# Kernel optimization log

Measured on AMD Instinct MI355X. Metric: run time of the kernel, lower is better.

Reference implementation:

```python
import jax, jax.numpy as jnp
import numpy as np

N, E = 50000, 800000
IN, HID, OUT, K = 500, 128, 128, 10
BN_EPS = 1e-5


def _encode(x, src, dst, norm, n, W_in, b_in, gam, high_pass, bn_scale, bn_shift, W_up, b_up):
    # input projection (dropout_p = 0 -> identity)
    h = x @ W_in + b_in  # [N, HID]

    def prop(t):
        # symmetric-normalized sparse matvec: (D^-1/2 A D^-1/2) t
        return jax.ops.segment_sum(norm[:, None] * t[src], dst, num_segments=n)

    def step(carry, g):
        t, acc = carry
        acc = acc + g * t
        pt = prop(t)
        # low-pass basis: A_hat^k x ; high-pass basis: (I - A_hat)^k x
        t = (t - pt) if high_pass else pt
        return (t, acc), None

    (_, acc), _ = jax.lax.scan(step, (h, jnp.zeros_like(h)), gam)

    # BatchNorm1d over the node axis (training-mode batch statistics)
    mu = acc.mean(axis=0)
    var = acc.var(axis=0)
    hn = (acc - mu) * jax.lax.rsqrt(var + BN_EPS) * bn_scale + bn_shift
    z = hn @ W_up + b_up
    return jax.nn.relu(z)  # act_fn='relu' (PolyGCL default)


def setup_inputs() -> dict:
    key = jax.random.key(0)
    ks = jax.random.split(key, 4)
    x = jax.random.normal(ks[0], (N, IN), dtype=jnp.float32)
    edge_index = jax.random.randint(ks[1], (2, E), 0, N, dtype=jnp.int32)
    W_in = jax.random.normal(ks[2], (IN, HID), dtype=jnp.float32) * (1.0 / np.sqrt(IN))
    b_in = jnp.zeros((HID,), dtype=jnp.float32)
    # low-pass: decreasing coefficients; high-pass: increasing (PolyGCL init scheme)
    gamma_L = jnp.linspace(2.0, 0.0, K + 1, dtype=jnp.float32)
    gamma_H = jnp.linspace(0.0, 2.0, K + 1, dtype=jnp.float32)
    bn_scale = jnp.ones((HID,), dtype=jnp.float32)
    bn_shift = jnp.zeros((HID,), dtype=jnp.float32)
    W_up = jax.random.normal(ks[3], (HID, OUT), dtype=jnp.float32) * (1.0 / np.sqrt(HID))
    b_up = jnp.zeros((OUT,), dtype=jnp.float32)
    return {"x": x, "edge_index": edge_index, "W_in": W_in, "b_in": b_in,
            "gamma_L": gamma_L, "gamma_H": gamma_H,
            "bn_scale": bn_scale, "bn_shift": bn_shift,
            "W_up": W_up, "b_up": b_up}


def reference(x, edge_index, W_in, b_in, gamma_L, gamma_H, bn_scale, bn_shift, W_up, b_up):
    n = x.shape[0]
    src, dst = edge_index[0], edge_index[1]
    deg = jax.ops.segment_sum(jnp.ones(src.shape, dtype=x.dtype), dst, num_segments=n)
    dinv = jax.lax.rsqrt(jnp.maximum(deg, 1.0))
    norm = dinv[src] * dinv[dst]  # [E]
    Z_L = _encode(x, src, dst, norm, n, W_in, b_in, gamma_L, False, bn_scale, bn_shift, W_up, b_up)
    Z_H = _encode(x, src, dst, norm, n, W_in, b_in, gamma_H, True, bn_scale, bn_shift, W_up, b_up)
    return (Z_L, Z_H)
```

## Files before the change

kernel.cpp:

```cpp
#include <hip/hip_runtime.h>
#include <hip/hip_fp16.h>

#define HIDF 128

typedef float v4f __attribute__((ext_vector_type(4)));
typedef _Float16 half8 __attribute__((ext_vector_type(8)));
typedef float f32x4 __attribute__((ext_vector_type(4)));
struct alignas(8) half4 { __half2 lo, hi; };

static inline int cdiv(int a, int b) { return (a + b - 1) / b; }
static inline size_t alup(size_t b) { return (b + 255) & ~(size_t)255; }

__global__ void k_deg(const int* __restrict__ dst, int E, int* __restrict__ deg) {
    int i = blockIdx.x * blockDim.x + threadIdx.x;
    if (i < E) atomicAdd(&deg[dst[i]], 1);
}

__global__ void k_coef(const float* __restrict__ gL, const float* __restrict__ gH, int K,
                       float* __restrict__ cL, float* __restrict__ cH) {
    if (threadIdx.x == 0 && blockIdx.x == 0) {
        for (int j = 0; j <= K; ++j) {
            double s = 0.0;
            double C = 1.0;
            for (int k = j; k <= K; ++k) {
                s += (double)gH[k] * C;
                C = C * (double)(k + 1) / (double)(k + 1 - j);
            }
            cH[j] = (j & 1) ? (float)(-s) : (float)s;
            cL[j] = gL[j];
        }
    }
}

__global__ __launch_bounds__(256) void k_scan1(const int* __restrict__ deg, int N,
                                               int* __restrict__ bsum,
                                               float* __restrict__ dinv) {
    __shared__ int ls[256];
    int tid = threadIdx.x;
    int i = blockIdx.x * 256 + tid;
    int v = 0;
    if (i < N) {
        v = deg[i];
        dinv[i] = rsqrtf(fmaxf((float)v, 1.0f));
    }
    ls[tid] = v;
    __syncthreads();
    for (int off = 128; off > 0; off >>= 1) {
        if (tid < off) ls[tid] += ls[tid + off];
        __syncthreads();
    }
    if (tid == 0) bsum[blockIdx.x] = ls[0];
}

__global__ __launch_bounds__(1024) void k_scan2(int* __restrict__ bsum, int nb) {
    __shared__ int ls[1024];
    int tid = threadIdx.x;
    int v = (tid < nb) ? bsum[tid] : 0;
    ls[tid] = v;
    __syncthreads();
    for (int off = 1; off < 1024; off <<= 1) {
        int t = (tid >= off) ? ls[tid - off] : 0;
        __syncthreads();
        ls[tid] += t;
        __syncthreads();
    }
    if (tid < nb) bsum[tid] = ls[tid] - v;
}

__global__ __launch_bounds__(256) void k_scan3(const int* __restrict__ deg,
                                               const int* __restrict__ bsum, int N,
                                               int* __restrict__ row_ptr) {
    __shared__ int ls[256];
    int tid = threadIdx.x;
    int i = blockIdx.x * 256 + tid;
    int v = (i < N) ? deg[i] : 0;
    ls[tid] = v;
    __syncthreads();
    for (int off = 1; off < 256; off <<= 1) {
        int t = (tid >= off) ? ls[tid - off] : 0;
        __syncthreads();
        ls[tid] += t;
        __syncthreads();
    }
    if (i <= N) row_ptr[i] = bsum[blockIdx.x] + ls[tid] - v;
}

__global__ __launch_bounds__(1024) void k_scan(const int* __restrict__ deg, int N,
                                               int* __restrict__ row_ptr,
                                               float* __restrict__ dinv) {
    __shared__ int ls[1024];
    int tid = threadIdx.x;
    int chunk = (N + 1023) / 1024;
    int start = tid * chunk;
    int end = min(start + chunk, N);
    int s = 0;
    for (int i = start; i < end; ++i) {
        int d = deg[i];
        s += d;
        dinv[i] = rsqrtf(fmaxf((float)d, 1.0f));
    }
    ls[tid] = s;
    __syncthreads();
    for (int off = 1; off < 1024; off <<= 1) {
        int v = (tid >= off) ? ls[tid - off] : 0;
        __syncthreads();
        ls[tid] += v;
        __syncthreads();
    }
    int run = ls[tid] - s;
    for (int i = start; i < end; ++i) {
        row_ptr[i] = run;
        run += deg[i];
    }
    if (tid == 1023) row_ptr[N] = run;
}

__global__ void k_scatter(const int* __restrict__ src, const int* __restrict__ dst, int E,
                          const int* __restrict__ row_ptr, int* __restrict__ fill,
                          const float* __restrict__ dinv, int* __restrict__ csr_src,
                          float* __restrict__ csr_w) {
    int i = blockIdx.x * blockDim.x + threadIdx.x;
    if (i < E) {
        int s = src[i], d = dst[i];
        int pos = row_ptr[d] + atomicAdd(&fill[d], 1);
        csr_src[pos] = s;
        csr_w[pos] = dinv[s] * dinv[d];
    }
}

__global__ __launch_bounds__(512) void k_wprep(const float* __restrict__ W, int Kdim, int KP,
                                               _Float16* __restrict__ Wh,
                                               _Float16* __restrict__ Wl) {
    int i = blockIdx.x * blockDim.x + threadIdx.x;
    int total = 128 * KP;
    if (i >= total) return;
    int n = i / KP;
    int k = i - n * KP;
    float w = (k < Kdim) ? W[(long)k * HIDF + n] : 0.0f;
    _Float16 h = (_Float16)w;
    _Float16 l = (_Float16)(w - (float)h);
    Wh[(long)n * KP + k] = h;
    Wl[(long)n * KP + k] = l;
}

__global__ __launch_bounds__(512) void k_gemm_in_mfma(
    const float* __restrict__ X, const _Float16* __restrict__ Wh,
    const _Float16* __restrict__ Wl, const float* __restrict__ b, __half* __restrict__ U0,
    int M, int Kdim, int KP) {
    __shared__ _Float16 Ah[128][40];
    __shared__ _Float16 Al[128][40];
    __shared__ _Float16 Bh[128][40];
    __shared__ _Float16 Bl[128][40];
    int tid = threadIdx.x;
    int lane = tid & 63;
    int wid = tid >> 6;
    int wr = wid >> 1;
    int wc = wid & 1;
    int lr = lane & 15;
    int kq = lane >> 4;
    int kof = kq * 8;
    int row0 = blockIdx.x * 128;
    int sm = tid >> 2;
    int kk = (tid & 3) * 8;
    bool k4ok = ((Kdim & 3) == 0);

    f32x4 acc[2][4] = {};

    for (int k0 = 0; k0 < KP; k0 += 32) {
        *(half8*)&Bh[sm][kk] = *(const half8*)&Wh[(long)sm * KP + k0 + kk];
        *(half8*)&Bl[sm][kk] = *(const half8*)&Wl[(long)sm * KP + k0 + kk];
        {
            int r = row0 + sm;
            int gk = k0 + kk;
            half8 hv, lv;
            if (r < M && (gk + 8) <= Kdim && k4ok) {
                float4 v0 = *(const float4*)&X[(long)r * Kdim + gk];
                float4 v1 = *(const float4*)&X[(long)r * Kdim + gk + 4];
                float xs[8] = {v0.x, v0.y, v0.z, v0.w, v1.x, v1.y, v1.z, v1.w};
#pragma unroll
                for (int j = 0; j < 8; ++j) {
                    _Float16 h = (_Float16)xs[j];
                    hv[j] = h;
                    lv[j] = (_Float16)(xs[j] - (float)h);
                }
            } else {
#pragma unroll
                for (int j = 0; j < 8; ++j) {
                    float x = (r < M && (gk + j) < Kdim) ? X[(long)r * Kdim + gk + j] : 0.0f;
                    _Float16 h = (_Float16)x;
                    hv[j] = h;
                    lv[j] = (_Float16)(x - (float)h);
                }
            }
            *(half8*)&Ah[sm][kk] = hv;
            *(half8*)&Al[sm][kk] = lv;
        }
        __syncthreads();

        half8 a_h0 = *(const half8*)&Ah[wr * 32 + lr][kof];
        half8 a_h1 = *(const half8*)&Ah[wr * 32 + 16 + lr][kof];
        half8 a_l0 = *(const half8*)&Al[wr * 32 + lr][kof];
        half8 a_l1 = *(const half8*)&Al[wr * 32 + 16 + lr][kof];
#pragma unroll
        for (int cg = 0; cg < 4; ++cg) {
            half8 b_h = *(const half8*)&Bh[wc * 64 + cg * 16 + lr][kof];
            half8 b_l = *(const half8*)&Bl[wc * 64 + cg * 16 + lr][kof];
            acc[0][cg] = __builtin_amdgcn_mfma_f32_16x16x32_f16(a_h0, b_h, acc[0][cg], 0, 0, 0);
            acc[1][cg] = __builtin_amdgcn_mfma_f32_16x16x32_f16(a_h1, b_h, acc[1][cg], 0, 0, 0);
            acc[0][cg] = __builtin_amdgcn_mfma_f32_16x16x32_f16(a_l0, b_h, acc[0][cg], 0, 0, 0);
            acc[1][cg] = __builtin_amdgcn_mfma_f32_16x16x32_f16(a_l1, b_h, acc[1][cg], 0, 0, 0);
            acc[0][cg] = __builtin_amdgcn_mfma_f32_16x16x32_f16(a_h0, b_l, acc[0][cg], 0, 0, 0);
            acc[1][cg] = __builtin_amdgcn_mfma_f32_16x16x32_f16(a_h1, b_l, acc[1][cg], 0, 0, 0);
        }
        __syncthreads();
    }

    float bb[4];
#pragma unroll
    for (int cg = 0; cg < 4; ++cg) bb[cg] = b[wc * 64 + cg * 16 + lr];
#pragma unroll
    for (int i = 0; i < 2; ++i) {
#pragma unroll
        for (int j = 0; j < 4; ++j) {
            int r = row0 + wr * 32 + i * 16 + kq * 4 + j;
            if (r < M) {
#pragma unroll
                for (int cg = 0; cg < 4; ++cg) {
                    int n = wc * 64 + cg * 16 + lr;
                    U0[(long)r * HIDF + n] = __float2half(acc[i][cg][j] + bb[cg]);
                }
            }
        }
    }
}

__global__ __launch_bounds__(512) void k_gemm_up_mfma(
    const float* __restrict__ accL, const float* __restrict__ accH,
    const _Float16* __restrict__ Wh, const _Float16* __restrict__ Wl,
    const float* __restrict__ bias, const float* __restrict__ a_mul,
    const float* __restrict__ aaW, float* __restrict__ out, int M) {
    int enc = blockIdx.y;
    const float* A = enc ? accH : accL;
    float* O = out + (size_t)enc * M * HIDF;
    __shared__ _Float16 Ah[128][40];
    __shared__ _Float16 Al[128][40];
    __shared__ _Float16 Bh[128][40];
    __shared__ _Float16 Bl[128][40];
    __shared__ float ams[128];
    int tid = threadIdx.x;
    int lane = tid & 63;
    int wid = tid >> 6;
    int wr = wid >> 1;
    int wc = wid & 1;
    int lr = lane & 15;
    int kq = lane >> 4;
    int kof = kq * 8;
    int row0 = blockIdx.x * 128;
    int sm = tid >> 2;
    int kk = (tid & 3) * 8;
    if (tid < 128) ams[tid] = a_mul[enc * 128 + tid];
    __syncthreads();

    f32x4 acc[2][4] = {};

    for (int k0 = 0; k0 < 128; k0 += 32) {
        *(half8*)&Bh[sm][kk] = *(const half8*)&Wh[(long)sm * 128 + k0 + kk];
        *(half8*)&Bl[sm][kk] = *(const half8*)&Wl[(long)sm * 128 + k0 + kk];
        {
            int r = row0 + sm;
            half8 hv, lv;
            if (r < M) {
                float4 v0 = *(const float4*)&A[(long)r * 128 + k0 + kk];
                float4 v1 = *(const float4*)&A[(long)r * 128 + k0 + kk + 4];
                float xs[8] = {v0.x, v0.y, v0.z, v0.w, v1.x, v1.y, v1.z, v1.w};
#pragma unroll
                for (int j = 0; j < 8; ++j) {
                    float sv = xs[j] * ams[k0 + kk + j];
                    _Float16 h = (_Float16)sv;
                    hv[j] = h;
                    lv[j] = (_Float16)(sv - (float)h);
                }
            } else {
#pragma unroll
                for (int j = 0; j < 8; ++j) { hv[j] = (_Float16)0.f; lv[j] = (_Float16)0.f; }
            }
            *(half8*)&Ah[sm][kk] = hv;
            *(half8*)&Al[sm][kk] = lv;
        }
        __syncthreads();

        half8 a_h0 = *(const half8*)&Ah[wr * 32 + lr][kof];
        half8 a_h1 = *(const half8*)&Ah[wr * 32 + 16 + lr][kof];
        half8 a_l0 = *(const half8*)&Al[wr * 32 + lr][kof];
        half8 a_l1 = *(const half8*)&Al[wr * 32 + 16 + lr][kof];
#pragma unroll
        for (int cg = 0; cg < 4; ++cg) {
            half8 b_h = *(const half8*)&Bh[wc * 64 + cg * 16 + lr][kof];
            half8 b_l = *(const half8*)&Bl[wc * 64 + cg * 16 + lr][kof];
            acc[0][cg] = __builtin_amdgcn_mfma_f32_16x16x32_f16(a_h0, b_h, acc[0][cg], 0, 0, 0);
            acc[1][cg] = __builtin_amdgcn_mfma_f32_16x16x32_f16(a_h1, b_h, acc[1][cg], 0, 0, 0);
            acc[0][cg] = __builtin_amdgcn_mfma_f32_16x16x32_f16(a_l0, b_h, acc[0][cg], 0, 0, 0);
            acc[1][cg] = __builtin_amdgcn_mfma_f32_16x16x32_f16(a_l1, b_h, acc[1][cg], 0, 0, 0);
            acc[0][cg] = __builtin_amdgcn_mfma_f32_16x16x32_f16(a_h0, b_l, acc[0][cg], 0, 0, 0);
            acc[1][cg] = __builtin_amdgcn_mfma_f32_16x16x32_f16(a_h1, b_l, acc[1][cg], 0, 0, 0);
        }
        __syncthreads();
    }

    float bb[4];
#pragma unroll
    for (int cg = 0; cg < 4; ++cg) {
        int n = wc * 64 + cg * 16 + lr;
        bb[cg] = bias[n] + aaW[enc * 128 + n];
    }
#pragma unroll
    for (int i = 0; i < 2; ++i) {
#pragma unroll
        for (int j = 0; j < 4; ++j) {
            int r = row0 + wr * 32 + i * 16 + kq * 4 + j;
            if (r < M) {
#pragma unroll
                for (int cg = 0; cg < 4; ++cg) {
                    int n = wc * 64 + cg * 16 + lr;
                    O[(long)r * HIDF + n] = fmaxf(acc[i][cg][j] + bb[cg], 0.0f);
                }
            }
        }
    }
}

__global__ __launch_bounds__(512) void k_gemm_in_f(
    const float* __restrict__ X, const float* __restrict__ W, const float* __restrict__ b,
    float* __restrict__ H, float* __restrict__ accL, float* __restrict__ accH,
    const float* __restrict__ cL, const float* __restrict__ cH, int M, int Kdim) {
    const int BK = 20;
    __shared__ float As[BK][132];
    __shared__ float Bs[BK][128];
    int tid = threadIdx.x;
    int tx = tid & 31, ty = tid >> 5;
    int row0 = blockIdx.x * 128;
    float acc[8][4] = {};
    for (int k0 = 0; k0 < Kdim; k0 += BK) {
        for (int l = tid; l < 640; l += 512) {
            int m = l / 5, q = l % 5;
            int r = row0 + m;
            float4 v = {0.f, 0.f, 0.f, 0.f};
            if (r < M) v = *(const float4*)&X[(long)r * Kdim + k0 + q * 4];
            As[q * 4 + 0][m] = v.x;
            As[q * 4 + 1][m] = v.y;
            As[q * 4 + 2][m] = v.z;
            As[q * 4 + 3][m] = v.w;
        }
        for (int l = tid; l < 640; l += 512) {
            int k = l >> 5, n = (l & 31) * 4;
            *(float4*)&Bs[k][n] = *(const float4*)&W[(long)(k0 + k) * 128 + n];
        }
        __syncthreads();
#pragma unroll
        for (int k = 0; k < BK; ++k) {
            float4 a0 = *(const float4*)&As[k][ty * 8];
            float4 a1 = *(const float4*)&As[k][ty * 8 + 4];
            float4 bb = *(const float4*)&Bs[k][tx * 4];
            float a[8] = {a0.x, a0.y, a0.z, a0.w, a1.x, a1.y, a1.z, a1.w};
#pragma unroll
            for (int i = 0; i < 8; ++i) {
                acc[i][0] += a[i] * bb.x;
                acc[i][1] += a[i] * bb.y;
                acc[i][2] += a[i] * bb.z;
                acc[i][3] += a[i] * bb.w;
            }
        }
        __syncthreads();
    }
    float g0 = cL[0], h0 = cH[0];
    float4 bias = *(const float4*)&b[tx * 4];
    float bv[4] = {bias.x, bias.y, bias.z, bias.w};
#pragma unroll
    for (int i = 0; i < 8; ++i) {
        int r = row0 + ty * 8 + i;
        if (r < M) {
            long idx = (long)r * 128 + tx * 4;
            float4 vh;
            float* ph = (float*)&vh;
#pragma unroll
            for (int j = 0; j < 4; ++j) ph[j] = acc[i][j] + bv[j];
            *(float4*)&H[idx] = vh;
            float4 vl = {g0 * vh.x, g0 * vh.y, g0 * vh.z, g0 * vh.w};
            float4 vv = {h0 * vh.x, h0 * vh.y, h0 * vh.z, h0 * vh.w};
            *(float4*)&accL[idx] = vl;
            *(float4*)&accH[idx] = vv;
        }
    }
}

__global__ __launch_bounds__(256) void k_prop_h(
    const int* __restrict__ row_ptr, const int* __restrict__ csr_src,
    const float* __restrict__ csr_w, const __half* __restrict__ t_in,
    __half* __restrict__ t_out, int N) {
    int tid = threadIdx.x;
    int lane = tid & 63;
    int wid = tid >> 6;
    int slot = lane >> 4;
    int l4 = lane & 15;
    int node = blockIdx.x * 16 + wid * 4 + slot;
    if (node >= N) return;
    int e0 = row_ptr[node], e1 = row_ptr[node + 1];
    float acc[8] = {};
    int e = e0;
    int nb = (e1 - e0) >> 3;

    int idxA[8];
    float wA[8];
    if (nb > 0) {
#pragma unroll
        for (int q = 0; q < 8; ++q) {
            idxA[q] = csr_src[e + q];
            wA[q] = csr_w[e + q];
        }
    }
    for (int bb = 0; bb < nb; ++bb) {
        half8 v[8];
#pragma unroll
        for (int q = 0; q < 8; ++q)
            v[q] = *(const half8*)&t_in[(long)idxA[q] * HIDF + l4 * 8];
        int en = e + 8;
        bool more = (bb + 1 < nb);
        int idxB[8];
        float wB[8];
        if (more) {
#pragma unroll
            for (int q = 0; q < 8; ++q) {
                idxB[q] = csr_src[en + q];
                wB[q] = csr_w[en + q];
            }
        }
#pragma unroll
        for (int q = 0; q < 8; ++q) {
#pragma unroll
            for (int f = 0; f < 8; ++f) acc[f] += wA[q] * (float)v[q][f];
        }
        if (more) {
#pragma unroll
            for (int q = 0; q < 8; ++q) {
                idxA[q] = idxB[q];
                wA[q] = wB[q];
            }
        }
        e = en;
    }
    for (; e < e1; ++e) {
        int i0 = csr_src[e];
        float w0 = csr_w[e];
        half8 v = *(const half8*)&t_in[(long)i0 * HIDF + l4 * 8];
#pragma unroll
        for (int f = 0; f < 8; ++f) acc[f] += w0 * (float)v[f];
    }
    half8 o;
#pragma unroll
    for (int f = 0; f < 8; ++f) o[f] = (_Float16)acc[f];
    *(half8*)&t_out[(long)node * HIDF + l4 * 8] = o;
}

__global__ __launch_bounds__(256) void k_prop(
    const int* __restrict__ row_ptr, const int* __restrict__ csr_src,
    const float* __restrict__ csr_w, const float* __restrict__ t_in,
    float* __restrict__ t_out, float* __restrict__ accL, float* __restrict__ accH,
    const float* __restrict__ cL, const float* __restrict__ cH, int j, int N, int write_t) {
    int wave = threadIdx.x >> 6;
    int lane = threadIdx.x & 63;
    int half = lane >> 5;
    int l5 = lane & 31;
    int node = blockIdx.x * 4 + wave;
    if (node >= N) return;
    int e0 = row_ptr[node], e1 = row_ptr[node + 1];
    float sx = 0.f, sy = 0.f, sz = 0.f, sw = 0.f;
    int e = e0 + half;
    for (; e + 6 < e1; e += 8) {
        int i0 = csr_src[e], i1 = csr_src[e + 2], i2 = csr_src[e + 4], i3 = csr_src[e + 6];
        float w0 = csr_w[e], w1 = csr_w[e + 2], w2 = csr_w[e + 4], w3 = csr_w[e + 6];
        float4 v0 = *(const float4*)&t_in[(long)i0 * HIDF + l5 * 4];
        float4 v1 = *(const float4*)&t_in[(long)i1 * HIDF + l5 * 4];
        float4 v2 = *(const float4*)&t_in[(long)i2 * HIDF + l5 * 4];
        float4 v3 = *(const float4*)&t_in[(long)i3 * HIDF + l5 * 4];
        sx += w0 * v0.x + w1 * v1.x + w2 * v2.x + w3 * v3.x;
        sy += w0 * v0.y + w1 * v1.y + w2 * v2.y + w3 * v3.y;
        sz += w0 * v0.z + w1 * v1.z + w2 * v2.z + w3 * v3.z;
        sw += w0 * v0.w + w1 * v1.w + w2 * v2.w + w3 * v3.w;
    }
    for (; e < e1; e += 2) {
        int i0 = csr_src[e];
        float w0 = csr_w[e];
        float4 v0 = *(const float4*)&t_in[(long)i0 * HIDF + l5 * 4];
        sx += w0 * v0.x;
        sy += w0 * v0.y;
        sz += w0 * v0.z;
        sw += w0 * v0.w;
    }
    sx += __shfl_xor(sx, 32);
    sy += __shfl_xor(sy, 32);
    sz += __shfl_xor(sz, 32);
    sw += __shfl_xor(sw, 32);
    if (half == 0) {
        long base = (long)node * HIDF + l5 * 4;
        if (write_t) {
            float4 o = {sx, sy, sz, sw};
            *(float4*)&t_out[base] = o;
        }
        float gL = cL[j], gH = cH[j];
        float4 aL = *(const float4*)&accL[base];
        float4 aH = *(const float4*)&accH[base];
        aL.x += gL * sx; aL.y += gL * sy; aL.z += gL * sz; aL.w += gL * sw;
        aH.x += gH * sx; aH.y += gH * sy; aH.z += gH * sz; aH.w += gH * sw;
        *(float4*)&accL[base] = aL;
        *(float4*)&accH[base] = aH;
    }
}

__global__ __launch_bounds__(256) void k_combine_h2(
    const __half* __restrict__ tb, long tstride, int K, float* __restrict__ accL,
    float* __restrict__ accH, const float* __restrict__ cL, const float* __restrict__ cH,
    int N, float* __restrict__ sums) {
    int tid = threadIdx.x;
    int fg = tid & 15;
    int rg = tid >> 4;
    int lane = tid & 63;
    int wid = tid >> 6;
    float s1[8] = {}, s2[8] = {}, s3[8] = {}, s4[8] = {};

    if (K == 10) {
        float gl[11], gh[11];
#pragma unroll
        for (int j = 0; j < 11; ++j) {
            gl[j] = cL[j];
            gh[j] = cH[j];
        }
        for (long r = (long)blockIdx.x * 16 + rg; r < N; r += (long)gridDim.x * 16) {
            const __half* p = tb + r * HIDF + fg * 8;
            half8 v[11];
#pragma unroll
            for (int j = 0; j < 11; ++j) v[j] = *(const half8*)(p + (long)j * tstride);
            float aL[8] = {}, aH[8] = {};
#pragma unroll
            for (int j = 0; j < 11; ++j) {
#pragma unroll
                for (int e = 0; e < 8; ++e) {
                    float t = (float)v[j][e];
                    aL[e] += gl[j] * t;
                    aH[e] += gh[j] * t;
                }
            }
            long base = r * HIDF + fg * 8;
            float4 o0 = {aL[0], aL[1], aL[2], aL[3]};
            float4 o1 = {aL[4], aL[5], aL[6], aL[7]};
            float4 o2 = {aH[0], aH[1], aH[2], aH[3]};
            float4 o3 = {aH[4], aH[5], aH[6], aH[7]};
            *(float4*)&accL[base] = o0;
            *(float4*)&accL[base + 4] = o1;
            *(float4*)&accH[base] = o2;
            *(float4*)&accH[base + 4] = o3;
#pragma unroll
            for (int e = 0; e < 8; ++e) {
                s1[e] += aL[e];
                s2[e] += aL[e] * aL[e];
                s3[e] += aH[e];
                s4[e] += aH[e] * aH[e];
            }
        }
    } else {
        for (long r = (long)blockIdx.x * 16 + rg; r < N; r += (long)gridDim.x * 16) {
            const __half* p = tb + r * HIDF + fg * 8;
            float aL[8] = {}, aH[8] = {};
            for (int j = 0; j <= K; ++j) {
                half8 v = *(const half8*)(p + (long)j * tstride);
                float gL = cL[j], gH = cH[j];
#pragma unroll
                for (int e = 0; e < 8; ++e) {
                    float t = (float)v[e];
                    aL[e] += gL * t;
                    aH[e] += gH * t;
                }
            }
            long base = r * HIDF + fg * 8;
            float4 o0 = {aL[0], aL[1], aL[2], aL[3]};
            float4 o1 = {aL[4], aL[5], aL[6], aL[7]};
            float4 o2 = {aH[0], aH[1], aH[2], aH[3]};
            float4 o3 = {aH[4], aH[5], aH[6], aH[7]};
            *(float4*)&accL[base] = o0;
            *(float4*)&accL[base + 4] = o1;
            *(float4*)&accH[base] = o2;
            *(float4*)&accH[base + 4] = o3;
#pragma unroll
            for (int e = 0; e < 8; ++e) {
                s1[e] += aL[e];
                s2[e] += aL[e] * aL[e];
                s3[e] += aH[e];
                s4[e] += aH[e] * aH[e];
            }
        }
    }

#pragma unroll
    for (int e = 0; e < 8; ++e) {
        s1[e] += __shfl_xor(s1[e], 16); s1[e] += __shfl_xor(s1[e], 32);
        s2[e] += __shfl_xor(s2[e], 16); s2[e] += __shfl_xor(s2[e], 32);
        s3[e] += __shfl_xor(s3[e], 16); s3[e] += __shfl_xor(s3[e], 32);
        s4[e] += __shfl_xor(s4[e], 16); s4[e] += __shfl_xor(s4[e], 32);
    }
    __shared__ float ls[4][16][32];
    if (lane < 16) {
#pragma unroll
        for (int e = 0; e < 8; ++e) {
            ls[wid][lane][e] = s1[e];
            ls[wid][lane][8 + e] = s2[e];
            ls[wid][lane][16 + e] = s3[e];
            ls[wid][lane][24 + e] = s4[e];
        }
    }
    __syncthreads();
    for (int idx = tid; idx < 512; idx += 256) {
        int f16i = idx >> 5, j = idx & 31;
        float v = ls[0][f16i][j] + ls[1][f16i][j] + ls[2][f16i][j] + ls[3][f16i][j];
        int stat = j >> 3, e = j & 7;
        atomicAdd(&sums[stat * 128 + f16i * 8 + e], v);
    }
}

__global__ __launch_bounds__(256) void k_stats(const float* __restrict__ accL,
                                               const float* __restrict__ accH, int N,
                                               float* __restrict__ sums) {
    int tid = threadIdx.x;
    int l5 = tid & 31;
    int g = tid >> 5;
    float4 l1 = {0, 0, 0, 0}, l2 = {0, 0, 0, 0}, h1 = {0, 0, 0, 0}, h2 = {0, 0, 0, 0};
    for (int r = blockIdx.x * 8 + g; r < N; r += gridDim.x * 8) {
        float4 v = *(const float4*)&accL[(long)r * HIDF + l5 * 4];
        l1.x += v.x; l1.y += v.y; l1.z += v.z; l1.w += v.w;
        l2.x += v.x * v.x; l2.y += v.y * v.y; l2.z += v.z * v.z; l2.w += v.w * v.w;
        float4 u = *(const float4*)&accH[(long)r * HIDF + l5 * 4];
        h1.x += u.x; h1.y += u.y; h1.z += u.z; h1.w += u.w;
        h2.x += u.x * u.x; h2.y += u.y * u.y; h2.z += u.z * u.z; h2.w += u.w * u.w;
    }
    __shared__ float4 s1[256], s2[256], s3[256], s4[256];
    s1[tid] = l1; s2[tid] = l2; s3[tid] = h1; s4[tid] = h2;
    __syncthreads();
    if (tid < 32) {
        float4 a = s1[tid], bq = s2[tid], c = s3[tid], d = s4[tid];
        for (int gg = 1; gg < 8; ++gg) {
            float4 t;
            t = s1[gg * 32 + tid]; a.x += t.x; a.y += t.y; a.z += t.z; a.w += t.w;
            t = s2[gg * 32 + tid]; bq.x += t.x; bq.y += t.y; bq.z += t.z; bq.w += t.w;
            t = s3[gg * 32 + tid]; c.x += t.x; c.y += t.y; c.z += t.z; c.w += t.w;
            t = s4[gg * 32 + tid]; d.x += t.x; d.y += t.y; d.z += t.z; d.w += t.w;
        }
        int f = tid * 4;
        atomicAdd(&sums[f + 0], a.x); atomicAdd(&sums[f + 1], a.y);
        atomicAdd(&sums[f + 2], a.z); atomicAdd(&sums[f + 3], a.w);
        atomicAdd(&sums[128 + f + 0], bq.x); atomicAdd(&sums[128 + f + 1], bq.y);
        atomicAdd(&sums[128 + f + 2], bq.z); atomicAdd(&sums[128 + f + 3], bq.w);
        atomicAdd(&sums[256 + f + 0], c.x); atomicAdd(&sums[256 + f + 1], c.y);
        atomicAdd(&sums[256 + f + 2], c.z); atomicAdd(&sums[256 + f + 3], c.w);
        atomicAdd(&sums[384 + f + 0], d.x); atomicAdd(&sums[384 + f + 1], d.y);
        atomicAdd(&sums[384 + f + 2], d.z); atomicAdd(&sums[384 + f + 3], d.w);
    }
}

__global__ void k_bnfin(const float* __restrict__ sums, int N, const float* __restrict__ scale,
                        const float* __restrict__ shift, const float* __restrict__ Wup,
                        float* __restrict__ a_mul, float* __restrict__ a_add,
                        float* __restrict__ aaW) {
    __shared__ float sh_add[2][128];
    int f = threadIdx.x;
    for (int enc = 0; enc < 2; ++enc) {
        float mu = sums[enc * 256 + f] / (float)N;
        float var = sums[enc * 256 + 128 + f] / (float)N - mu * mu;
        float rstd = rsqrtf(var + 1e-5f);
        float am = rstd * scale[f];
        a_mul[enc * 128 + f] = am;
        float ad = shift[f] - mu * am;
        a_add[enc * 128 + f] = ad;
        sh_add[enc][f] = ad;
    }
    __syncthreads();
    int n = f;
    float s0 = 0.f, s1 = 0.f;
    for (int ff = 0; ff < 128; ++ff) {
        float w = Wup[ff * 128 + n];
        s0 += sh_add[0][ff] * w;
        s1 += sh_add[1][ff] * w;
    }
    aaW[n] = s0;
    aaW[128 + n] = s1;
}

extern "C" void kernel_launch(void* const* d_in, const int* in_sizes, int n_in, void* d_out,
                              int out_size, void* d_ws, size_t ws_size, hipStream_t stream) {
    const float* x = (const float*)d_in[0];
    const int* edge_index = (const int*)d_in[1];
    const float* W_in = (const float*)d_in[2];
    const float* b_in = (const float*)d_in[3];
    const float* gamma_L = (const float*)d_in[4];
    const float* gamma_H = (const float*)d_in[5];
    const float* bn_scale = (const float*)d_in[6];
    const float* bn_shift = (const float*)d_in[7];
    const float* W_up = (const float*)d_in[8];
    const float* b_up = (const float*)d_in[9];
    float* out = (float*)d_out;

    const int HID = in_sizes[3];
    const int IN = in_sizes[2] / HID;
    const int N = in_sizes[0] / IN;
    const int E = in_sizes[1] / 2;
    const int K = in_sizes[4] - 1;

    const int* src = edge_index;
    const int* dst = edge_index + E;

    const int KP = (IN + 31) & ~31;

    char* base = (char*)d_ws;
    size_t off = 0;
    auto take = [&](size_t bytes) -> char* {
        char* r = base + off;
        off += alup(bytes);
        return r;
    };
    int* deg = (int*)take((size_t)N * 4);
    int* row_ptr = (int*)take((size_t)(N + 1) * 4);
    int* fill = (int*)take((size_t)N * 4);
    float* dinv = (float*)take((size_t)N * 4);
    int* bsum = (int*)take(1024 * 4);
    int* csr_src = (int*)take((size_t)E * 4);
    float* csr_w = (float*)take((size_t)E * 4);
    float* accL = (float*)take((size_t)N * HID * 4);
    float* accH = (float*)take((size_t)N * HID * 4);
    float* sums = (float*)take(512 * 4);
    float* cL = (float*)take(64 * 4);
    float* cH = (float*)take(64 * 4);
    float* a_mul = (float*)take(256 * 4);
    float* a_add = (float*)take(256 * 4);
    float* aaW = (float*)take(256 * 4);
    _Float16* Wt_h = (_Float16*)take((size_t)HID * KP * 2);
    _Float16* Wt_l = (_Float16*)take((size_t)HID * KP * 2);
    _Float16* Wup_h = (_Float16*)take((size_t)HID * HID * 2);
    _Float16* Wup_l = (_Float16*)take((size_t)HID * HID * 2);

    size_t per16 = alup((size_t)N * HID * 2);
    long stride16 = (long)(per16 / 2);
    __half* tb16 = (__half*)(base + off);
    bool deferred = (off + (size_t)(K + 1) * per16) <= ws_size && K < 60;
    size_t per32 = alup((size_t)N * HID * 4);
    long stride32 = (long)(per32 / 4);
    float* fb = (float*)(base + off);
    if (!deferred && off + 2 * per32 > ws_size) deferred = true;

    hipMemsetAsync(deg, 0, (size_t)N * 4, stream);
    hipMemsetAsync(fill, 0, (size_t)N * 4, stream);
    hipMemsetAsync(sums, 0, 512 * 4, stream);

    k_coef<<<1, 64, 0, stream>>>(gamma_L, gamma_H, K, cL, cH);
    k_deg<<<cdiv(E, 256), 256, 0, stream>>>(dst, E, deg);

    int nb = cdiv(N + 1, 256);
    if (nb <= 1024) {
        k_scan1<<<nb, 256, 0, stream>>>(deg, N, bsum, dinv);
        k_scan2<<<1, 1024, 0, stream>>>(bsum, nb);
        k_scan3<<<nb, 256, 0, stream>>>(deg, bsum, N, row_ptr);
    } else {
        k_scan<<<1, 1024, 0, stream>>>(deg, N, row_ptr, dinv);
    }

    k_scatter<<<cdiv(E, 256), 256, 0, stream>>>(src, dst, E, row_ptr, fill, dinv, csr_src,
                                                csr_w);
    k_wprep<<<cdiv(HID * HID, 512), 512, 0, stream>>>(W_up, HID, HID, Wup_h, Wup_l);

    if (deferred) {
        k_wprep<<<cdiv(HID * KP, 512), 512, 0, stream>>>(W_in, IN, KP, Wt_h, Wt_l);
        k_gemm_in_mfma<<<cdiv(N, 128), 512, 0, stream>>>(x, Wt_h, Wt_l, b_in, tb16, N, IN, KP);
        for (int j = 1; j <= K; ++j) {
            const __half* tin = tb16 + (long)(j - 1) * stride16;
            __half* tout = tb16 + (long)j * stride16;
            k_prop_h<<<cdiv(N, 16), 256, 0, stream>>>(row_ptr, csr_src, csr_w, tin, tout, N);
        }
        k_combine_h2<<<512, 256, 0, stream>>>(tb16, stride16, K, accL, accH, cL, cH, N, sums);
    } else {
        float* h = fb;
        float* ta = fb + stride32;
        k_gemm_in_f<<<cdiv(N, 128), 512, 0, stream>>>(x, W_in, b_in, h, accL, accH, cL, cH,
                                                      N, IN);
        const float* tin = h;
        float* tout = ta;
        for (int j = 1; j <= K; ++j) {
            int write_t = (j < K) ? 1 : 0;
            k_prop<<<cdiv(N, 4), 256, 0, stream>>>(row_ptr, csr_src, csr_w, tin, tout, accL,
                                                   accH, cL, cH, j, N, write_t);
            const float* nt = tout;
            tout = (nt == ta) ? h : ta;
            tin = nt;
        }
        k_stats<<<200, 256, 0, stream>>>(accL, accH, N, sums);
    }

    k_bnfin<<<1, 128, 0, stream>>>(sums, N, bn_scale, bn_shift, W_up, a_mul, a_add, aaW);
    dim3 gup(cdiv(N, 128), 2);
    k_gemm_up_mfma<<<gup, 512, 0, stream>>>(accL, accH, Wup_h, Wup_l, b_up, a_mul, aaW, out,
                                            N);
}
```

Baseline: 720.2 us.

## Split fp16 propagation over feature quarters and prefetch GEMM tiles in registers

```diff
diff --git a/kernel.cpp b/kernel.cpp
--- a/kernel.cpp
+++ b/kernel.cpp
@@ -163,40 +163,41 @@
     int sm = tid >> 2;
     int kk = (tid & 3) * 8;
     bool k4ok = ((Kdim & 3) == 0);
+    int r_st = row0 + sm;
 
     f32x4 acc[2][4] = {};
-
-    for (int k0 = 0; k0 < KP; k0 += 32) {
-        *(half8*)&Bh[sm][kk] = *(const half8*)&Wh[(long)sm * KP + k0 + kk];
-        *(half8*)&Bl[sm][kk] = *(const half8*)&Wl[(long)sm * KP + k0 + kk];
-        {
-            int r = row0 + sm;
-            int gk = k0 + kk;
-            half8 hv, lv;
-            if (r < M && (gk + 8) <= Kdim && k4ok) {
-                float4 v0 = *(const float4*)&X[(long)r * Kdim + gk];
-                float4 v1 = *(const float4*)&X[(long)r * Kdim + gk + 4];
-                float xs[8] = {v0.x, v0.y, v0.z, v0.w, v1.x, v1.y, v1.z, v1.w};
-#pragma unroll
-                for (int j = 0; j < 8; ++j) {
-                    _Float16 h = (_Float16)xs[j];
-                    hv[j] = h;
-                    lv[j] = (_Float16)(xs[j] - (float)h);
-                }
-            } else {
-#pragma unroll
-                for (int j = 0; j < 8; ++j) {
-                    float x = (r < M && (gk + j) < Kdim) ? X[(long)r * Kdim + gk + j] : 0.0f;
-                    _Float16 h = (_Float16)x;
-                    hv[j] = h;
-                    lv[j] = (_Float16)(x - (float)h);
-                }
-            }
-            *(half8*)&Ah[sm][kk] = hv;
-            *(half8*)&Al[sm][kk] = lv;
-        }
-        __syncthreads();
-
+    float xs[8];
+    half8 wbh, wbl;
+
+    auto LOAD = [&](int k0) {
+        wbh = *(const half8*)&Wh[(long)sm * KP + k0 + kk];
+        wbl = *(const half8*)&Wl[(long)sm * KP + k0 + kk];
+        int gk = k0 + kk;
+        if (r_st < M && k4ok && (gk + 8) <= Kdim) {
+            float4 v0 = *(const float4*)&X[(long)r_st * Kdim + gk];
+            float4 v1 = *(const float4*)&X[(long)r_st * Kdim + gk + 4];
+            xs[0] = v0.x; xs[1] = v0.y; xs[2] = v0.z; xs[3] = v0.w;
+            xs[4] = v1.x; xs[5] = v1.y; xs[6] = v1.z; xs[7] = v1.w;
+        } else {
+#pragma unroll
+            for (int j = 0; j < 8; ++j)
+                xs[j] = (r_st < M && (gk + j) < Kdim) ? X[(long)r_st * Kdim + gk + j] : 0.0f;
+        }
+    };
+    auto WRITE = [&]() {
+        half8 hv, lv;
+#pragma unroll
+        for (int j = 0; j < 8; ++j) {
+            _Float16 h = (_Float16)xs[j];
+            hv[j] = h;
+            lv[j] = (_Float16)(xs[j] - (float)h);
+        }
+        *(half8*)&Ah[sm][kk] = hv;
+        *(half8*)&Al[sm][kk] = lv;
+        *(half8*)&Bh[sm][kk] = wbh;
+        *(half8*)&Bl[sm][kk] = wbl;
+    };
+    auto COMPUTE = [&]() {
         half8 a_h0 = *(const half8*)&Ah[wr * 32 + lr][kof];
         half8 a_h1 = *(const half8*)&Ah[wr * 32 + 16 + lr][kof];
         half8 a_l0 = *(const half8*)&Al[wr * 32 + lr][kof];
@@ -212,7 +213,20 @@
             acc[0][cg] = __builtin_amdgcn_mfma_f32_16x16x32_f16(a_h0, b_l, acc[0][cg], 0, 0, 0);
             acc[1][cg] = __builtin_amdgcn_mfma_f32_16x16x32_f16(a_h1, b_l, acc[1][cg], 0, 0, 0);
         }
-        __syncthreads();
+    };
+
+    const int NT = KP / 32;
+    LOAD(0);
+    WRITE();
+    __syncthreads();
+    for (int t = 0; t < NT; ++t) {
+        if (t + 1 < NT) LOAD((t + 1) * 32);
+        COMPUTE();
+        __syncthreads();
+        if (t + 1 < NT) {
+            WRITE();
+            __syncthreads();
+        }
     }
 
     float bb[4];
@@ -393,72 +407,54 @@
     }
 }
 
-__global__ __launch_bounds__(256) void k_prop_h(
+__global__ __launch_bounds__(256) void k_prop_hp(
     const int* __restrict__ row_ptr, const int* __restrict__ csr_src,
     const float* __restrict__ csr_w, const __half* __restrict__ t_in,
     __half* __restrict__ t_out, int N) {
+    int p = blockIdx.y;
     int tid = threadIdx.x;
     int lane = tid & 63;
     int wid = tid >> 6;
-    int slot = lane >> 4;
-    int l4 = lane & 15;
-    int node = blockIdx.x * 16 + wid * 4 + slot;
+    int slot = lane >> 3;
+    int fl = lane & 7;
+    int node = blockIdx.x * 4 + wid;
     if (node >= N) return;
     int e0 = row_ptr[node], e1 = row_ptr[node + 1];
-    float acc[8] = {};
-    int e = e0;
-    int nb = (e1 - e0) >> 3;
-
-    int idxA[8];
-    float wA[8];
-    if (nb > 0) {
-#pragma unroll
-        for (int q = 0; q < 8; ++q) {
-            idxA[q] = csr_src[e + q];
-            wA[q] = csr_w[e + q];
-        }
-    }
-    for (int bb = 0; bb < nb; ++bb) {
-        half8 v[8];
-#pragma unroll
-        for (int q = 0; q < 8; ++q)
-            v[q] = *(const half8*)&t_in[(long)idxA[q] * HIDF + l4 * 8];
-        int en = e + 8;
-        bool more = (bb + 1 < nb);
-        int idxB[8];
-        float wB[8];
-        if (more) {
-#pragma unroll
-            for (int q = 0; q < 8; ++q) {
-                idxB[q] = csr_src[en + q];
-                wB[q] = csr_w[en + q];
-            }
-        }
-#pragma unroll
-        for (int q = 0; q < 8; ++q) {
-#pragma unroll
-            for (int f = 0; f < 8; ++f) acc[f] += wA[q] * (float)v[q][f];
-        }
-        if (more) {
-#pragma unroll
-            for (int q = 0; q < 8; ++q) {
-                idxA[q] = idxB[q];
-                wA[q] = wB[q];
-            }
-        }
-        e = en;
-    }
-    for (; e < e1; ++e) {
+    const __half* tp = t_in + p * 32 + fl * 4;
+    float a0 = 0.f, a1 = 0.f, a2 = 0.f, a3 = 0.f;
+    int e = e0 + slot;
+    for (; e + 8 < e1; e += 16) {
+        int i0 = csr_src[e], i1 = csr_src[e + 8];
+        float w0 = csr_w[e], w1 = csr_w[e + 8];
+        half4 v0 = *(const half4*)&tp[(long)i0 * HIDF];
+        half4 v1 = *(const half4*)&tp[(long)i1 * HIDF];
+        float2 x0 = __half22float2(v0.lo), y0 = __half22float2(v0.hi);
+        float2 x1 = __half22float2(v1.lo), y1 = __half22float2(v1.hi);
+        a0 += w0 * x0.x + w1 * x1.x;
+        a1 += w0 * x0.y + w1 * x1.y;
+        a2 += w0 * y0.x + w1 * y1.x;
+        a3 += w0 * y0.y + w1 * y1.y;
+    }
+    if (e < e1) {
         int i0 = csr_src[e];
         float w0 = csr_w[e];
-        half8 v = *(const half8*)&t_in[(long)i0 * HIDF + l4 * 8];
-#pragma unroll
-        for (int f = 0; f < 8; ++f) acc[f] += w0 * (float)v[f];
-    }
-    half8 o;
-#pragma unroll
-    for (int f = 0; f < 8; ++f) o[f] = (_Float16)acc[f];
-    *(half8*)&t_out[(long)node * HIDF + l4 * 8] = o;
+        half4 v0 = *(const half4*)&tp[(long)i0 * HIDF];
+        float2 x0 = __half22float2(v0.lo), y0 = __half22float2(v0.hi);
+        a0 += w0 * x0.x;
+        a1 += w0 * x0.y;
+        a2 += w0 * y0.x;
+        a3 += w0 * y0.y;
+    }
+    a0 += __shfl_xor(a0, 8); a0 += __shfl_xor(a0, 16); a0 += __shfl_xor(a0, 32);
+    a1 += __shfl_xor(a1, 8); a1 += __shfl_xor(a1, 16); a1 += __shfl_xor(a1, 32);
+    a2 += __shfl_xor(a2, 8); a2 += __shfl_xor(a2, 16); a2 += __shfl_xor(a2, 32);
+    a3 += __shfl_xor(a3, 8); a3 += __shfl_xor(a3, 16); a3 += __shfl_xor(a3, 32);
+    if (slot == 0) {
+        half4 o;
+        o.lo = __float22half2_rn(make_float2(a0, a1));
+        o.hi = __float22half2_rn(make_float2(a2, a3));
+        *(half4*)&t_out[(long)node * HIDF + p * 32 + fl * 4] = o;
+    }
 }
 
 __global__ __launch_bounds__(256) void k_prop(
@@ -747,11 +743,10 @@
     size_t per16 = alup((size_t)N * HID * 2);
     long stride16 = (long)(per16 / 2);
     __half* tb16 = (__half*)(base + off);
-    bool deferred = (off + (size_t)(K + 1) * per16) <= ws_size && K < 60;
+    bool deferred = (off + (size_t)(K + 1) * per16) <= ws_size && K < 60 && (HID == 128);
     size_t per32 = alup((size_t)N * HID * 4);
     long stride32 = (long)(per32 / 4);
     float* fb = (float*)(base + off);
-    if (!deferred && off + 2 * per32 > ws_size) deferred = true;
 
     hipMemsetAsync(deg, 0, (size_t)N * 4, stream);
     hipMemsetAsync(fill, 0, (size_t)N * 4, stream);
@@ -776,10 +771,11 @@
     if (deferred) {
         k_wprep<<<cdiv(HID * KP, 512), 512, 0, stream>>>(W_in, IN, KP, Wt_h, Wt_l);
         k_gemm_in_mfma<<<cdiv(N, 128), 512, 0, stream>>>(x, Wt_h, Wt_l, b_in, tb16, N, IN, KP);
+        dim3 gp(cdiv(N, 4), HIDF / 32);
         for (int j = 1; j <= K; ++j) {
             const __half* tin = tb16 + (long)(j - 1) * stride16;
             __half* tout = tb16 + (long)j * stride16;
-            k_prop_h<<<cdiv(N, 16), 256, 0, stream>>>(row_ptr, csr_src, csr_w, tin, tout, N);
+            k_prop_hp<<<gp, 256, 0, stream>>>(row_ptr, csr_src, csr_w, tin, tout, N);
         }
         k_combine_h2<<<512, 256, 0, stream>>>(tb16, stride16, K, accL, accH, cL, cH, N, sums);
     } else {
```

Measured after the change: 1.016 ms. +41.1%, slower.
